# Performance work log

Measured on AMD Instinct MI355X. Metric: run time of the kernel, lower is better.

## Reference

```python
import jax, jax.numpy as jnp
import numpy as np

NHEAD = 16
D_MODEL = 1024
DK = D_MODEL // NHEAD
Q_DIM = V_DIM = K_DIM = 1024
B, S = 2, 2048


def _xavier(key, shape):
    # xavier_uniform over last two dims (fan_in=shape[-2], fan_out=shape[-1])
    fan_in, fan_out = shape[-2], shape[-1]
    limit = float(np.sqrt(6.0 / (fan_in + fan_out)))
    return jax.random.uniform(key, shape, jnp.float32, -limit, limit)


def setup_inputs() -> dict:
    key = jax.random.key(0)
    kq, kv, kk, kwq, kwv, kwk = jax.random.split(key, 6)
    q = jax.random.normal(kq, (B, S, Q_DIM), jnp.float32)
    v = jax.random.normal(kv, (B, S, V_DIM), jnp.float32)
    k = jax.random.normal(kk, (B, S, K_DIM), jnp.float32)
    # causal mask: True = attend, matches masked_fill(~mask, -inf)
    causal = jnp.tril(jnp.ones((S, S), dtype=bool))
    attn_mask = jnp.broadcast_to(causal, (B, S, S))
    q_proj_mats = _xavier(kwq, (NHEAD, Q_DIM, DK))
    v_proj_mats = _xavier(kwv, (NHEAD, V_DIM, DK))
    k_proj_mats = _xavier(kwk, (NHEAD, K_DIM, DK))
    return {"q": q, "v": v, "k": k, "attn_mask": attn_mask,
            "q_proj_mats": q_proj_mats, "v_proj_mats": v_proj_mats,
            "k_proj_mats": k_proj_mats}


def reference(q, v, k, attn_mask, q_proj_mats, v_proj_mats, k_proj_mats):
    bsz, seq_len, _ = q.shape
    # per-head projections: [B,S,dim] x [H,dim,dk] -> [B,H,S,dk]
    qp = jnp.einsum('bsk,hkd->bhsd', q, q_proj_mats)
    vp = jnp.einsum('bsk,hkd->bhsd', v, v_proj_mats)
    kp = jnp.einsum('bsk,hkd->bhsd', k, k_proj_mats)
    # NOTE: original scales by sqrt(d_model), not sqrt(dk)
    scale = 1.0 / jnp.sqrt(jnp.float32(D_MODEL))
    logits = jnp.einsum('bhqd,bhkd->bhqk', qp, kp) * scale  # [B,H,S,S]
    logits = jnp.where(attn_mask[:, None, :, :], logits, -jnp.inf)
    score = jax.nn.softmax(logits, axis=-1)
    weighted = jnp.einsum('bhkd,bhqk->bqhd', vp, score)  # [B,S,H,dk]
    return weighted.reshape(bsz, seq_len, -1)
```

## Files before the change

kernel.cpp:

```cpp
#include <hip/hip_runtime.h>
#include <cstdint>
#include <cstddef>

#define NB 2
#define NS 2048
#define NH 16
#define NDK 64
#define NDM 1024
#define SCALE 0.03125f
#define QSCALE 0.045084220f

using u16 = unsigned short;
typedef __attribute__((ext_vector_type(8))) short bf16x8;
typedef __attribute__((ext_vector_type(4))) short bf16x4;
typedef __attribute__((ext_vector_type(4))) float f32x4;

#define AS1 __attribute__((address_space(1)))
#define AS3 __attribute__((address_space(3)))

__device__ __forceinline__ u16 f2bf(float f) {
    unsigned int x = __float_as_uint(f);
    return (u16)((x + 0x7FFFu + ((x >> 16) & 1u)) >> 16);
}
__device__ __forceinline__ unsigned int packbf(float f0, float f1) {
    return __builtin_amdgcn_perm(__float_as_uint(f1), __float_as_uint(f0),
                                 0x07060302u);
}
__device__ __forceinline__ float fexp2(float x) {
#if defined(__HIP_DEVICE_COMPILE__) && __has_builtin(__builtin_amdgcn_exp2f)
    return __builtin_amdgcn_exp2f(x);
#else
    return __builtin_exp2f(x);
#endif
}
__device__ __forceinline__ f32x4 mfma16(bf16x4 a, bf16x4 b, f32x4 c) {
#if !defined(__HIP_DEVICE_COMPILE__)
    (void)a; (void)b;
    return c;
#elif __has_builtin(__builtin_amdgcn_mfma_f32_16x16x16bf16_1k)
    return __builtin_amdgcn_mfma_f32_16x16x16bf16_1k(a, b, c, 0, 0, 0);
#else
    typedef __attribute__((ext_vector_type(4))) __bf16 bf16v4;
    return __builtin_amdgcn_mfma_f32_16x16x16_bf16(
        *reinterpret_cast<bf16v4*>(&a), *reinterpret_cast<bf16v4*>(&b),
        c, 0, 0, 0);
#endif
}

__global__ __launch_bounds__(256)
void prep(const float* __restrict__ q, const float* __restrict__ v,
          const float* __restrict__ kkk,
          const float* __restrict__ qw, const float* __restrict__ vw,
          const float* __restrict__ kw,
          u16* __restrict__ xt, u16* __restrict__ wbt, int nxblk)
{
    __shared__ __align__(16) u16 SH[64 * 72];
    const int t = threadIdx.x;
    const int bid = blockIdx.x;
    if (bid < nxblk) {
        int z   = bid >> 7;
        int rem = bid & 127;
        int mt  = rem >> 2;
        int kq  = rem & 3;
        const float* X = (z == 0) ? q : (z == 1) ? v : kkk;
        const float* src = X + (size_t)mt * 128 * NDM;
        u16* dst = xt + (((size_t)z * 32 + mt) << 17);
        const int row = t >> 3;
        const int cl  = (t & 7) * 4;
        const int pl  = (t & 7) >> 1;
        const int hf  = (t & 1) * 4;
        for (int kk = kq * 8; kk < kq * 8 + 8; ++kk) {
            #pragma unroll
            for (int i = 0; i < 4; ++i) {
                int ml = row + 32 * i;
                float4 f = *reinterpret_cast<const float4*>(
                    src + (size_t)ml * NDM + kk * 32 + cl);
                uint2 u;
                u.x = packbf(f.x, f.y);
                u.y = packbf(f.z, f.w);
                *reinterpret_cast<uint2*>(&SH[(pl * 128 + ml) * 8 + hf]) = u;
            }
            __syncthreads();
            {
                uint4 o0 = *reinterpret_cast<uint4*>(&SH[(2 * t) * 8]);
                uint4 o1 = *reinterpret_cast<uint4*>(&SH[(2 * t + 1) * 8]);
                u16* dd = dst + ((size_t)kk << 12) + 2 * t * 8;
                *reinterpret_cast<uint4*>(dd)     = o0;
                *reinterpret_cast<uint4*>(dd + 8) = o1;
            }
            __syncthreads();
        }
    } else {
        int b  = bid - nxblk;
        int z  = b >> 8;
        int h  = (b >> 4) & 15;
        int k0 = (b & 15) * 64;
        const float* W = ((z == 0) ? qw : (z == 1) ? vw : kw)
                         + (size_t)h * NDM * NDK;
        {
            int kr = t >> 2, d0 = (t & 3) * 16;
            const float* src = W + (size_t)(k0 + kr) * NDK + d0;
            #pragma unroll
            for (int c = 0; c < 4; ++c) {
                float4 f = *reinterpret_cast<const float4*>(src + c * 4);
                SH[(d0 + c * 4 + 0) * 72 + kr] = f2bf(f.x);
                SH[(d0 + c * 4 + 1) * 72 + kr] = f2bf(f.y);
                SH[(d0 + c * 4 + 2) * 72 + kr] = f2bf(f.z);
                SH[(d0 + c * 4 + 3) * 72 + kr] = f2bf(f.w);
            }
        }
        __syncthreads();
        {
            int pl = t >> 6, d = t & 63;
            int nt = h >> 1;
            int cb = pl * 128 + (h & 1) * 64 + d;
            #pragma unroll
            for (int ki = 0; ki < 2; ++ki) {
                uint4 val = *reinterpret_cast<const uint4*>(
                    &SH[d * 72 + ki * 32 + pl * 8]);
                size_t base = (((size_t)z * 8 + nt) * 32 + (k0 >> 5) + ki) << 12;
                *reinterpret_cast<uint4*>(wbt + base + cb * 8) = val;
            }
        }
    }
}

__device__ __forceinline__ void gemm_epilogue(
    f32x4 acc[4][4], int z, int m0, int n0, int wm, int wn,
    int quad, int l15, u16* __restrict__ O)
{
    const int bb = m0 >> 11;
    const int hh = (n0 + wn) >> 6;
    const size_t headT = ((size_t)(bb * NH + hh)) << 17;
    if (z == 2) {
        #pragma unroll
        for (int mi = 0; mi < 4; ++mi) {
            #pragma unroll
            for (int r = 0; r < 4; ++r) {
                int s = (m0 + wm + mi * 16 + quad * 4 + r) & 2047;
                size_t tb = headT + ((size_t)(s >> 6) << 12) + (s & 63) * 8 + (l15 & 7);
                int chb = l15 >> 3;
                #pragma unroll
                for (int ni = 0; ni < 4; ++ni)
                    O[tb + (ni * 2 + chb) * 512] = f2bf(acc[mi][ni][r]);
            }
        }
    } else if (z == 1) {
        #pragma unroll
        for (int mi = 0; mi < 4; ++mi) {
            #pragma unroll
            for (int r = 0; r < 4; ++r) {
                int s = (m0 + wm + mi * 16 + quad * 4 + r) & 2047;
                size_t tb = headT + ((size_t)(s >> 6) << 12)
                          + ((s & 63) >> 3) * 512 + (s & 7);
                #pragma unroll
                for (int ni = 0; ni < 4; ++ni)
                    O[tb + (ni * 16 + l15) * 8] = f2bf(acc[mi][ni][r]);
            }
        }
    } else {
        #pragma unroll
        for (int mi = 0; mi < 4; ++mi) {
            #pragma unroll
            for (int r = 0; r < 4; ++r) {
                int s = (m0 + wm + mi * 16 + quad * 4 + r) & 2047;
                size_t rb = ((size_t)(bb * NH + hh) * NS + s) * NDK;
                #pragma unroll
                for (int ni = 0; ni < 4; ++ni)
                    O[rb + ni * 16 + l15] = f2bf(acc[mi][ni][r] * QSCALE);
            }
        }
    }
}

#define GSTEP(KK, CUR, PRE, ISSUE, VMC)                                        \
    {                                                                          \
        asm volatile("s_waitcnt vmcnt(" #VMC ")" ::: "memory");                \
        __builtin_amdgcn_s_barrier();                                          \
        __builtin_amdgcn_sched_barrier(0);                                     \
        if (ISSUE) {                                                           \
            const size_t off_ = (size_t)((KK) + 2) << 12;                      \
            _Pragma("unroll")                                                  \
            for (int i_ = 0; i_ < 2; ++i_) {                                   \
                int c_ = i_ * 256 + t;                                         \
                __builtin_amdgcn_global_load_lds(                              \
                    (const AS1 void*)(As + off_ + c_ * 8),                     \
                    (AS3 void*)&SA[PRE][c_ * 8], 16, 0, 0);                    \
                __builtin_amdgcn_global_load_lds(                              \
                    (const AS1 void*)(Bs + off_ + c_ * 8),                     \
                    (AS3 void*)&SB[PRE][c_ * 8], 16, 0, 0);                    \
            }                                                                  \
        }                                                                      \
        bf16x8 af_[4], bf_[4];                                                 \
        _Pragma("unroll")                                                      \
        for (int mi_ = 0; mi_ < 4; ++mi_)                                      \
            af_[mi_] = *reinterpret_cast<const bf16x8*>(                       \
                &SA[CUR][quad * 1024 + (wm + mi_ * 16 + l15) * 8]);            \
        _Pragma("unroll")                                                      \
        for (int ni_ = 0; ni_ < 4; ++ni_)                                      \
            bf_[ni_] = *reinterpret_cast<const bf16x8*>(                       \
                &SB[CUR][quad * 1024 + (wn + ni_ * 16 + l15) * 8]);            \
        _Pragma("unroll")                                                      \
        for (int mi_ = 0; mi_ < 4; ++mi_)                                      \
            _Pragma("unroll")                                                  \
            for (int ni_ = 0; ni_ < 4; ++ni_)                                  \
                acc[mi_][ni_] = __builtin_amdgcn_mfma_f32_16x16x32_bf16(       \
                    af_[mi_], bf_[ni_], acc[mi_][ni_], 0, 0, 0);               \
    }

__global__ __launch_bounds__(256)
void gemm_xt(const u16* __restrict__ xt, const u16* __restrict__ wbt,
             u16* __restrict__ qp, u16* __restrict__ vp,
             u16* __restrict__ kp)
{
    __shared__ __align__(16) u16 SA[3][4096];
    __shared__ __align__(16) u16 SB[3][4096];

    const int t    = threadIdx.x;
    const int lane = t & 63;
    const int w    = t >> 6;
    const int quad = lane >> 4, l15 = lane & 15;
    const int mt = blockIdx.x, nt = blockIdx.y, z = blockIdx.z;

    const u16* As = xt + (((size_t)z * 32 + mt) << 17);
    const u16* Bs = wbt + (((size_t)z * 8 + nt) << 17);
    u16* O = (z == 0) ? qp : (z == 1) ? vp : kp;
    const int wm = (w & 1) * 64, wn = (w >> 1) * 64;

    #pragma unroll
    for (int i = 0; i < 2; ++i) {
        int c = i * 256 + t;
        __builtin_amdgcn_global_load_lds((const AS1 void*)(As + c * 8),
                                         (AS3 void*)&SA[0][c * 8], 16, 0, 0);
        __builtin_amdgcn_global_load_lds((const AS1 void*)(Bs + c * 8),
                                         (AS3 void*)&SB[0][c * 8], 16, 0, 0);
    }
    #pragma unroll
    for (int i = 0; i < 2; ++i) {
        int c = i * 256 + t;
        __builtin_amdgcn_global_load_lds((const AS1 void*)(As + 4096 + c * 8),
                                         (AS3 void*)&SA[1][c * 8], 16, 0, 0);
        __builtin_amdgcn_global_load_lds((const AS1 void*)(Bs + 4096 + c * 8),
                                         (AS3 void*)&SB[1][c * 8], 16, 0, 0);
    }

    f32x4 acc[4][4] = {};

    for (int kk = 0; kk < 30; kk += 3) {
        GSTEP(kk + 0, 0, 2, true, 4);
        GSTEP(kk + 1, 1, 0, true, 4);
        GSTEP(kk + 2, 2, 1, true, 4);
    }
    GSTEP(30, 0, 2, false, 4);
    GSTEP(31, 1, 0, false, 0);

    gemm_epilogue(acc, z, mt * 128, nt * 128, wm, wn, quad, l15, O);
}
#undef GSTEP

__global__ __launch_bounds__(256)
void gemm_pack(const float* __restrict__ q, const float* __restrict__ v,
               const float* __restrict__ kkk, const u16* __restrict__ wbt,
               u16* __restrict__ qp, u16* __restrict__ vp,
               u16* __restrict__ kp)
{
    __shared__ __align__(16) u16 SA[2][4096];
    __shared__ __align__(16) u16 SB[2][4096];

    const int t    = threadIdx.x;
    const int lane = t & 63;
    const int w    = t >> 6;
    const int quad = lane >> 4, l15 = lane & 15;
    const int m0 = blockIdx.x * 128;
    const int n0 = blockIdx.y * 128;
    const int z  = blockIdx.z;

    const float* X = (z == 0) ? q : (z == 1) ? v : kkk;
    const u16* Wb2 = wbt + (((size_t)z * 8 + (n0 >> 7)) << 17);
    u16* O = (z == 0) ? qp : (z == 1) ? vp : kp;

    const int wm = (w & 1) * 64, wn = (w >> 1) * 64;
    const int arow = t >> 3;
    const int acol = (t & 7) * 4;
    const int apl  = (t & 7) >> 1;
    const int aj   = (t & 1) * 4;
    const float* xa = X + (size_t)(m0 + arow) * NDM + acol;

    float4 fA[4];
    #pragma unroll
    for (int i = 0; i < 4; ++i)
        fA[i] = *reinterpret_cast<const float4*>(xa + (size_t)(32 * i) * NDM);
    #pragma unroll
    for (int i = 0; i < 2; ++i) {
        int c = i * 256 + t;
        __builtin_amdgcn_global_load_lds((const AS1 void*)(Wb2 + c * 8),
                                         (AS3 void*)&SB[0][c * 8], 16, 0, 0);
    }

    f32x4 acc[4][4] = {};

    #pragma unroll 2
    for (int kk = 0; kk < 32; ++kk) {
        const int cur = kk & 1;
        #pragma unroll
        for (int i = 0; i < 4; ++i) {
            uint2 u;
            u.x = packbf(fA[i].x, fA[i].y);
            u.y = packbf(fA[i].z, fA[i].w);
            *reinterpret_cast<uint2*>(
                &SA[cur][apl * 1024 + (arow + 32 * i) * 8 + aj]) = u;
        }
        __syncthreads();

        if (kk < 31) {
            const int kn = (kk + 1) * 32;
            const float* p = xa + kn;
            #pragma unroll
            for (int i = 0; i < 4; ++i)
                fA[i] = *reinterpret_cast<const float4*>(p + (size_t)(32 * i) * NDM);
            const u16* src = Wb2 + ((size_t)(kk + 1) << 12);
            #pragma unroll
            for (int i = 0; i < 2; ++i) {
                int c = i * 256 + t;
                __builtin_amdgcn_global_load_lds((const AS1 void*)(src + c * 8),
                                                 (AS3 void*)&SB[cur ^ 1][c * 8], 16, 0, 0);
            }
        }

        bf16x8 af[4], bfr[4];
        #pragma unroll
        for (int mi = 0; mi < 4; ++mi)
            af[mi] = *reinterpret_cast<const bf16x8*>(
                &SA[cur][quad * 1024 + (wm + mi * 16 + l15) * 8]);
        #pragma unroll
        for (int ni = 0; ni < 4; ++ni)
            bfr[ni] = *reinterpret_cast<const bf16x8*>(
                &SB[cur][quad * 1024 + (wn + ni * 16 + l15) * 8]);
        #pragma unroll
        for (int mi = 0; mi < 4; ++mi)
            #pragma unroll
            for (int ni = 0; ni < 4; ++ni)
                acc[mi][ni] = __builtin_amdgcn_mfma_f32_16x16x32_bf16(
                    af[mi], bfr[ni], acc[mi][ni], 0, 0, 0);
    }

    gemm_epilogue(acc, z, m0, n0, wm, wn, quad, l15, O);
}

__global__ __launch_bounds__(256, 3)
void attn_kernel(const u16* __restrict__ QP, const u16* __restrict__ KP,
                 const u16* __restrict__ VT, float* __restrict__ Out)
{
    __shared__ __align__(16) u16 SMEM[16384];
    __shared__ float LS[4][4][16];

    u16* KB = SMEM;
    u16* VB = SMEM + 8192;

    const int t    = threadIdx.x;
    const int w    = t >> 6;
    const int lane = t & 63;
    const int quad = lane >> 4, l15 = lane & 15;

    const int qt = 31 - (blockIdx.x >> 5);
    const int bh = blockIdx.x & 31;
    const size_t headQ = (size_t)bh * NS * NDK;
    const size_t headT = (size_t)bh << 17;
    const int q0 = qt * 64;

    bf16x8 qf[4][2];
    #pragma unroll
    for (int qg = 0; qg < 4; ++qg) {
        const u16* qa = QP + headQ + (size_t)(q0 + qg * 16 + l15) * NDK + quad * 8;
        qf[qg][0] = *reinterpret_cast<const bf16x8*>(qa);
        qf[qg][1] = *reinterpret_cast<const bf16x8*>(qa + 32);
    }

    f32x4 o[4][4] = {};
    float ls[4] = {};

    #pragma unroll
    for (int i = 0; i < 2; ++i) {
        int c = i * 256 + t;
        __builtin_amdgcn_global_load_lds((const AS1 void*)(KP + headT + c * 8),
                                         (AS3 void*)&KB[c * 8], 16, 0, 0);
        __builtin_amdgcn_global_load_lds((const AS1 void*)(VT + headT + c * 8),
                                         (AS3 void*)&VB[c * 8], 16, 0, 0);
    }

    for (int kt = 0; kt <= qt; ++kt) {
        const int cur = kt & 1;
        __syncthreads();
        if (kt < qt) {
            const size_t tb = headT + ((size_t)(kt + 1) << 12);
            const int nb = cur ^ 1;
            #pragma unroll
            for (int i = 0; i < 2; ++i) {
                int c = i * 256 + t;
                __builtin_amdgcn_global_load_lds((const AS1 void*)(KP + tb + c * 8),
                                                 (AS3 void*)&KB[nb * 4096 + c * 8], 16, 0, 0);
                __builtin_amdgcn_global_load_lds((const AS1 void*)(VT + tb + c * 8),
                                                 (AS3 void*)&VB[nb * 4096 + c * 8], 16, 0, 0);
            }
        }
        const u16* KBc = KB + cur * 4096;
        const u16* VBc = VB + cur * 4096;

        bf16x8 k0 = *reinterpret_cast<const bf16x8*>(
            &KBc[quad * 512 + (w * 16 + l15) * 8]);
        bf16x8 k1 = *reinterpret_cast<const bf16x8*>(
            &KBc[(quad + 4) * 512 + (w * 16 + l15) * 8]);

        const bool diag = (kt == qt);
        bf16x4 pf[4];
        #pragma unroll
        for (int qg = 0; qg < 4; ++qg) {
            f32x4 z = {};
            f32x4 s = __builtin_amdgcn_mfma_f32_16x16x32_bf16(k1, qf[qg][1],
                        __builtin_amdgcn_mfma_f32_16x16x32_bf16(k0, qf[qg][0], z, 0, 0, 0),
                        0, 0, 0);
            float p0 = fexp2(s[0]);
            float p1 = fexp2(s[1]);
            float p2 = fexp2(s[2]);
            float p3 = fexp2(s[3]);
            if (diag) {
                const int kb = w * 16 + quad * 4;
                const int qr = qg * 16 + l15;
                if (kb + 0 > qr) p0 = 0.0f;
                if (kb + 1 > qr) p1 = 0.0f;
                if (kb + 2 > qr) p2 = 0.0f;
                if (kb + 3 > qr) p3 = 0.0f;
            }
            ls[qg] += (p0 + p1) + (p2 + p3);
            union { unsigned int u[2]; bf16x4 v; } pu;
            pu.u[0] = packbf(p0, p1);
            pu.u[1] = packbf(p2, p3);
            pf[qg] = pu.v;
        }

        #pragma unroll
        for (int d = 0; d < 4; ++d) {
            const bf16x4 vf = *reinterpret_cast<const bf16x4*>(
                &VBc[(2 * w + (quad >> 1)) * 512 + (d * 16 + l15) * 8 + (quad & 1) * 4]);
            #pragma unroll
            for (int qg = 0; qg < 4; ++qg)
                o[qg][d] = mfma16(pf[qg], vf, o[qg][d]);
        }
    }

    #pragma unroll
    for (int qg = 0; qg < 4; ++qg) {
        ls[qg] += __shfl_xor(ls[qg], 16, 64);
        ls[qg] += __shfl_xor(ls[qg], 32, 64);
    }

    __syncthreads();
    if (quad == 0) {
        #pragma unroll
        for (int qg = 0; qg < 4; ++qg) LS[w][qg][l15] = ls[qg];
    }
    __syncthreads();
    float inv[4];
    #pragma unroll
    for (int qg = 0; qg < 4; ++qg)
        inv[qg] = 1.0f / (LS[0][qg][l15] + LS[1][qg][l15]
                        + LS[2][qg][l15] + LS[3][qg][l15]);

    float* SC = reinterpret_cast<float*>(SMEM);
    const int bb = bh >> 4, h = bh & 15;
    #pragma unroll
    for (int round = 0; round < 2; ++round) {
        const int qgA = round * 2, qgB = round * 2 + 1;
        if (w != qgA) {
            #pragma unroll
            for (int d = 0; d < 4; ++d)
                *reinterpret_cast<f32x4*>(
                    SC + ((qgA & 1) * 4 + w) * 1024 + (d * 16 + l15) * 16 + quad * 4)
                    = o[qgA][d];
        }
        if (w != qgB) {
            #pragma unroll
            for (int d = 0; d < 4; ++d)
                *reinterpret_cast<f32x4*>(
                    SC + ((qgB & 1) * 4 + w) * 1024 + (d * 16 + l15) * 16 + quad * 4)
                    = o[qgB][d];
        }
        __syncthreads();
        if (w == qgA || w == qgB) {
            const int qg = w;
            const float invq = (w == qgA) ? inv[qgA] : inv[qgB];
            f32x4 acc[4];
            #pragma unroll
            for (int d = 0; d < 4; ++d) {
                acc[d] = (w == qgA) ? o[qgA][d] : o[qgB][d];
                #pragma unroll
                for (int w2 = 0; w2 < 4; ++w2) {
                    if (w2 != qg)
                        acc[d] += *reinterpret_cast<const f32x4*>(
                            SC + ((qg & 1) * 4 + w2) * 1024
                               + (d * 16 + l15) * 16 + quad * 4);
                }
            }
            #pragma unroll
            for (int r = 0; r < 4; ++r) {
                const float iv = __shfl(invq, quad * 4 + r, 64);
                const size_t ob = ((size_t)bb * NS + q0 + qg * 16 + quad * 4 + r)
                                  * NDM + h * 64 + l15;
                #pragma unroll
                for (int d = 0; d < 4; ++d)
                    Out[ob + d * 16] = acc[d][r] * iv;
            }
        }
        if (round == 0) __syncthreads();
    }
}

extern "C" void kernel_launch(void* const* d_in, const int* in_sizes, int n_in,
                              void* d_out, int out_size, void* d_ws, size_t ws_size,
                              hipStream_t stream) {
    const float* q  = (const float*)d_in[0];
    const float* v  = (const float*)d_in[1];
    const float* k  = (const float*)d_in[2];
    const float* qw = (const float*)d_in[4];
    const float* vw = (const float*)d_in[5];
    const float* kw = (const float*)d_in[6];

    const size_t PSZ = (size_t)NB * NH * NS * NDK;
    u16* wbt = (u16*)d_ws;
    u16* qp  = wbt + (size_t)3 * NDM * NDM;
    u16* vp  = qp + PSZ;
    u16* kp  = vp + PSZ;
    u16* xt  = kp + PSZ;

    const size_t NEED_XT = ((size_t)3 * NDM * NDM + 3 * PSZ
                            + (size_t)3 * 4096 * NDM) * 2;
    const bool xtpath = (ws_size >= NEED_XT);
    const int nx = xtpath ? 384 : 0;

    prep<<<dim3(768 + nx), dim3(256), 0, stream>>>(
        q, v, k, qw, vw, kw, xtpath ? xt : (u16*)d_ws, wbt, nx);

    if (xtpath)
        gemm_xt<<<dim3(32, 8, 3), dim3(256), 0, stream>>>(xt, wbt, qp, vp, kp);
    else
        gemm_pack<<<dim3(32, 8, 3), dim3(256), 0, stream>>>(q, v, k, wbt,
                                                            qp, vp, kp);

    attn_kernel<<<dim3(32 * 32), dim3(256), 0, stream>>>(qp, kp, vp,
                                                         (float*)d_out);
}
```

Measured before the change: 204.4 us.

## Load B operand directly into registers instead of staging through LDS

In the projection GEMM, the weight (B) tiles are no longer staged through shared memory. Each wave now loads its B fragments straight from global memory into a triple-buffered register array, one k-step ahead. Only A keeps the LDS pipeline, and the vmcnt waits are retuned to match. This halves LDS use and removes the B LDS reads, and launch bounds now request 3 blocks per CU. The cost is extra registers and duplicated global loads of B across the waves that share the same wn. There is also the risk that the register prefetch is not hidden behind the MFMA work.

```diff
diff --git a/kernel.cpp b/kernel.cpp
--- a/kernel.cpp
+++ b/kernel.cpp
@@ -173,12 +173,20 @@
     }
 }
 
-#define GSTEP(KK, CUR, PRE, ISSUE, VMC)                                        \
+#define GSTEP(KK, CUR, NXT, PRE, VMA, DO_B, DO_A)                              \
     {                                                                          \
-        asm volatile("s_waitcnt vmcnt(" #VMC ")" ::: "memory");                \
+        asm volatile("s_waitcnt vmcnt(" #VMA ")" ::: "memory");                \
         __builtin_amdgcn_s_barrier();                                          \
         __builtin_amdgcn_sched_barrier(0);                                     \
-        if (ISSUE) {                                                           \
+        if (DO_B) {                                                            \
+            const u16* bsrc_ = Bs + ((size_t)((KK) + 1) << 12)                 \
+                             + (quad * 128 + wn + l15) * 8;                    \
+            _Pragma("unroll")                                                  \
+            for (int ni_ = 0; ni_ < 4; ++ni_)                                  \
+                breg[NXT][ni_] = *reinterpret_cast<const bf16x8*>(             \
+                    bsrc_ + ni_ * 128);                                        \
+        }                                                                      \
+        if (DO_A) {                                                            \
             const size_t off_ = (size_t)((KK) + 2) << 12;                      \
             _Pragma("unroll")                                                  \
             for (int i_ = 0; i_ < 2; ++i_) {                                   \
@@ -186,35 +194,28 @@
                 __builtin_amdgcn_global_load_lds(                              \
                     (const AS1 void*)(As + off_ + c_ * 8),                     \
                     (AS3 void*)&SA[PRE][c_ * 8], 16, 0, 0);                    \
-                __builtin_amdgcn_global_load_lds(                              \
-                    (const AS1 void*)(Bs + off_ + c_ * 8),                     \
-                    (AS3 void*)&SB[PRE][c_ * 8], 16, 0, 0);                    \
             }                                                                  \
         }                                                                      \
-        bf16x8 af_[4], bf_[4];                                                 \
+        __builtin_amdgcn_sched_barrier(0);                                     \
+        bf16x8 af_[4];                                                         \
         _Pragma("unroll")                                                      \
         for (int mi_ = 0; mi_ < 4; ++mi_)                                      \
             af_[mi_] = *reinterpret_cast<const bf16x8*>(                       \
                 &SA[CUR][quad * 1024 + (wm + mi_ * 16 + l15) * 8]);            \
         _Pragma("unroll")                                                      \
-        for (int ni_ = 0; ni_ < 4; ++ni_)                                      \
-            bf_[ni_] = *reinterpret_cast<const bf16x8*>(                       \
-                &SB[CUR][quad * 1024 + (wn + ni_ * 16 + l15) * 8]);            \
-        _Pragma("unroll")                                                      \
         for (int mi_ = 0; mi_ < 4; ++mi_)                                      \
             _Pragma("unroll")                                                  \
             for (int ni_ = 0; ni_ < 4; ++ni_)                                  \
                 acc[mi_][ni_] = __builtin_amdgcn_mfma_f32_16x16x32_bf16(       \
-                    af_[mi_], bf_[ni_], acc[mi_][ni_], 0, 0, 0);               \
-    }
-
-__global__ __launch_bounds__(256)
+                    af_[mi_], breg[CUR][ni_], acc[mi_][ni_], 0, 0, 0);         \
+    }
+
+__global__ __launch_bounds__(256, 3)
 void gemm_xt(const u16* __restrict__ xt, const u16* __restrict__ wbt,
              u16* __restrict__ qp, u16* __restrict__ vp,
              u16* __restrict__ kp)
 {
     __shared__ __align__(16) u16 SA[3][4096];
-    __shared__ __align__(16) u16 SB[3][4096];
 
     const int t    = threadIdx.x;
     const int lane = t & 63;
@@ -227,32 +228,36 @@
     u16* O = (z == 0) ? qp : (z == 1) ? vp : kp;
     const int wm = (w & 1) * 64, wn = (w >> 1) * 64;
 
+    bf16x8 breg[3][4];
+
     #pragma unroll
     for (int i = 0; i < 2; ++i) {
         int c = i * 256 + t;
         __builtin_amdgcn_global_load_lds((const AS1 void*)(As + c * 8),
                                          (AS3 void*)&SA[0][c * 8], 16, 0, 0);
-        __builtin_amdgcn_global_load_lds((const AS1 void*)(Bs + c * 8),
-                                         (AS3 void*)&SB[0][c * 8], 16, 0, 0);
+    }
+    {
+        const u16* bsrc = Bs + (quad * 128 + wn + l15) * 8;
+        #pragma unroll
+        for (int ni = 0; ni < 4; ++ni)
+            breg[0][ni] = *reinterpret_cast<const bf16x8*>(bsrc + ni * 128);
     }
     #pragma unroll
     for (int i = 0; i < 2; ++i) {
         int c = i * 256 + t;
         __builtin_amdgcn_global_load_lds((const AS1 void*)(As + 4096 + c * 8),
                                          (AS3 void*)&SA[1][c * 8], 16, 0, 0);
-        __builtin_amdgcn_global_load_lds((const AS1 void*)(Bs + 4096 + c * 8),
-                                         (AS3 void*)&SB[1][c * 8], 16, 0, 0);
     }
 
     f32x4 acc[4][4] = {};
 
     for (int kk = 0; kk < 30; kk += 3) {
-        GSTEP(kk + 0, 0, 2, true, 4);
-        GSTEP(kk + 1, 1, 0, true, 4);
-        GSTEP(kk + 2, 2, 1, true, 4);
-    }
-    GSTEP(30, 0, 2, false, 4);
-    GSTEP(31, 1, 0, false, 0);
+        GSTEP(kk + 0, 0, 1, 2, 6, true, true);
+        GSTEP(kk + 1, 1, 2, 0, 6, true, true);
+        GSTEP(kk + 2, 2, 0, 1, 6, true, true);
+    }
+    GSTEP(30, 0, 1, 2, 6, true, false);
+    GSTEP(31, 1, 2, 0, 4, false, false);
 
     gemm_epilogue(acc, z, mt * 128, nt * 128, wm, wn, quad, l15, O);
 }
```

Measured after the change: 190.6 us. 1.07x faster.
